# Performance work log

Measured on AMD Instinct MI355X. Metric: run time of the kernel, lower is better.

Reference implementation:

```python
import jax, jax.numpy as jnp
import numpy as np

# Dimensions
O, D, F_LSOA = 128, 128, 64      # origins, destinations, LSOA feature dim
T, FE, H = 128, 16, 64           # max seq len, edge_feature_dim, gru_hidden
NH, NO, PH = 128, 64, 128        # node_hidden, node_out, pair_hidden
P = O * D                        # number of O-D pairs


def _mlp3(x, W1, b1, W2, b2, W3, b3):
    # Linear->ReLU->Linear->ReLU->Linear (dropout is identity in eval mode)
    h = jax.nn.relu(x @ W1 + b1)
    h = jax.nn.relu(h @ W2 + b2)
    return h @ W3 + b3


def setup_inputs() -> dict:
    key = jax.random.key(0)
    ks = jax.random.split(key, 32)

    def rn(k, shape, s):
        return jax.random.normal(k, shape, dtype=jnp.float32) * s

    inp = {
        "O_feats": rn(ks[0], (O, F_LSOA), 1.0),
        "D_feats": rn(ks[1], (D, F_LSOA), 1.0),
        "seqs": rn(ks[2], (P, T, FE), 1.0),
        "lengths": jax.random.randint(ks[3], (P,), 1, T + 1, dtype=jnp.int32),
        # enc_O
        "WO1": rn(ks[4], (F_LSOA, NH), 0.05), "bO1": jnp.zeros((NH,), jnp.float32),
        "WO2": rn(ks[5], (NH, NH), 0.05),     "bO2": jnp.zeros((NH,), jnp.float32),
        "WO3": rn(ks[6], (NH, NO), 0.05),     "bO3": jnp.zeros((NO,), jnp.float32),
        # enc_D
        "WD1": rn(ks[7], (F_LSOA, NH), 0.05), "bD1": jnp.zeros((NH,), jnp.float32),
        "WD2": rn(ks[8], (NH, NH), 0.05),     "bD2": jnp.zeros((NH,), jnp.float32),
        "WD3": rn(ks[9], (NH, NO), 0.05),     "bD3": jnp.zeros((NO,), jnp.float32),
        # pair_head: 2*node_out -> pair_hidden -> 1
        "Wp1": rn(ks[10], (2 * NO, PH), 0.05), "bp1": jnp.zeros((PH,), jnp.float32),
        "Wp2": rn(ks[11], (PH, 1), 0.05),      "bp2": jnp.zeros((1,), jnp.float32),
        # GRU (gate order r, z, n as in PyTorch)
        "W_ih": rn(ks[12], (FE, 3 * H), 0.1),  "b_ih": jnp.zeros((3 * H,), jnp.float32),
        "W_hh": rn(ks[13], (H, 3 * H), 0.1),   "b_hh": jnp.zeros((3 * H,), jnp.float32),
        # seq_head
        "Ws": rn(ks[14], (H, 1), 0.1),         "bs": jnp.zeros((1,), jnp.float32),
    }
    return inp


def reference(O_feats, D_feats, seqs, lengths,
              WO1, bO1, WO2, bO2, WO3, bO3,
              WD1, bD1, WD2, bD2, WD3, bD3,
              Wp1, bp1, Wp2, bp2,
              W_ih, W_hh, b_ih, b_hh,
              Ws, bs):
    # Node encoders
    eo = _mlp3(O_feats, WO1, bO1, WO2, bO2, WO3, bO3)   # [O, NO]
    ed = _mlp3(D_feats, WD1, bD1, WD2, bD2, WD3, bD3)   # [D, NO]

    # Pairwise score: concat(eo, ed) -> MLP -> softplus
    pair_in = jnp.concatenate([
        jnp.broadcast_to(eo[:, None, :], (O, D, NO)),
        jnp.broadcast_to(ed[None, :, :], (O, D, NO)),
    ], axis=-1)                                          # [O, D, 2*NO]
    hp = jax.nn.relu(pair_in @ Wp1 + bp1)                # [O, D, PH]
    z_pair = (hp @ Wp2 + bp2)[..., 0]                    # [O, D]
    s_pair = jax.nn.softplus(z_pair)

    # Length-masked GRU over all O*D padded sequences (equiv. to pack_padded)
    xT = jnp.swapaxes(seqs, 0, 1)                        # [T, P, FE]
    h0 = jnp.zeros((P, H), jnp.float32)

    def step(h, inp):
        xt, t = inp
        gx = xt @ W_ih + b_ih                            # [P, 3H]
        gh = h @ W_hh + b_hh                             # [P, 3H]
        xr, xz, xn = jnp.split(gx, 3, axis=-1)
        hr, hz, hn = jnp.split(gh, 3, axis=-1)
        r = jax.nn.sigmoid(xr + hr)
        zg = jax.nn.sigmoid(xz + hz)
        n = jnp.tanh(xn + r * hn)
        h_new = (1.0 - zg) * n + zg * h
        h = jnp.where((t < lengths)[:, None], h_new, h)  # freeze past seq end
        return h, None

    h_last, _ = jax.lax.scan(step, h0, (xT, jnp.arange(T)))  # [P, H]

    p_seq = jax.nn.sigmoid(h_last @ Ws + bs)[:, 0].reshape(O, D)
    return jnp.sum(s_pair * p_seq)
```

## Files before the change

### kernel.cpp

```cpp
#include <hip/hip_runtime.h>
#include <hip/hip_bf16.h>

#define O_N 128
#define D_N 128
#define F_LS 64
#define T_MAX 128
#define FE_N 16
#define H_GRU 64
#define NH 128
#define NO 64
#define PH 128
#define NGRP 1024

typedef _Float16 f16;
typedef __fp16 hf2 __attribute__((ext_vector_type(2)));
typedef f16 f16x4 __attribute__((ext_vector_type(4)));
typedef f16 f16x8 __attribute__((ext_vector_type(8)));
typedef float f32x4 __attribute__((ext_vector_type(4)));

__device__ __forceinline__ float fast_sigmoid(float x) {
    return __builtin_amdgcn_rcpf(1.f + __expf(-x));
}

__global__ __launch_bounds__(256) void k_pre(
    const float* __restrict__ O_feats, const float* __restrict__ D_feats,
    const float* __restrict__ WO1, const float* __restrict__ bO1,
    const float* __restrict__ WO2, const float* __restrict__ bO2,
    const float* __restrict__ WO3, const float* __restrict__ bO3,
    const float* __restrict__ WD1, const float* __restrict__ bD1,
    const float* __restrict__ WD2, const float* __restrict__ bD2,
    const float* __restrict__ WD3, const float* __restrict__ bD3,
    const float* __restrict__ Wp1, const float* __restrict__ bp1,
    const int* __restrict__ lengths,
    float* __restrict__ PA, float* __restrict__ PBt,
    int* __restrict__ perm, int* __restrict__ gcnt, float* __restrict__ d_out)
{
    const int t = threadIdx.x;
    if (blockIdx.x == 256) {
        __shared__ int cnt[130];
        __shared__ int suf[130];
        if (t == 0) gcnt[0] = 0;
        if (t < 130) cnt[t] = 0;
        __syncthreads();
        for (int i = t; i < 16384; i += 256) atomicAdd(&cnt[lengths[i]], 1);
        __syncthreads();
        if (t < 130) suf[t] = cnt[t];
        __syncthreads();
        for (int d = 1; d < 130; d <<= 1) {
            int v = 0;
            if (t < 130) { v = suf[t]; if (t + d < 130) v += suf[t + d]; }
            __syncthreads();
            if (t < 130) suf[t] = v;
            __syncthreads();
        }
        if (t < 129) cnt[t] = (t + 1 < 130) ? suf[t + 1] : 0;
        __syncthreads();
        for (int i = t; i < 16384; i += 256) {
            int pos = atomicAdd(&cnt[lengths[i]], 1);
            perm[pos] = i;
        }
        return;
    }

    __shared__ float h1[NH];
    __shared__ float h2[NH];
    __shared__ float ev[NO];
    const int b = blockIdx.x;
    const int enc = b >> 7;
    const int row = b & 127;
    if (b == 0 && t == 0) d_out[0] = 0.f;

    const float* x  = (enc ? D_feats : O_feats) + row * F_LS;
    const float* W1 = enc ? WD1 : WO1;  const float* b1 = enc ? bD1 : bO1;
    const float* W2 = enc ? WD2 : WO2;  const float* b2 = enc ? bD2 : bO2;
    const float* W3 = enc ? WD3 : WO3;  const float* b3 = enc ? bD3 : bO3;

    if (t < 128) {
        float a = b1[t];
        #pragma unroll 8
        for (int k = 0; k < F_LS; ++k) a += x[k] * W1[k * NH + t];
        h1[t] = fmaxf(a, 0.f);
    }
    __syncthreads();

    if (t < 128) {
        float a = b2[t];
        #pragma unroll 8
        for (int k = 0; k < NH; ++k) a += h1[k] * W2[k * NH + t];
        h2[t] = fmaxf(a, 0.f);
    }
    __syncthreads();

    if (t < NO) {
        float a = b3[t];
        #pragma unroll 8
        for (int k = 0; k < NH; ++k) a += h2[k] * W3[k * NO + t];
        ev[t] = a;
    }
    __syncthreads();

    if (t < 128) {
        const float* Wp = Wp1 + (enc ? NO * PH : 0);
        float a = 0.f;
        #pragma unroll 8
        for (int k = 0; k < NO; ++k) a += ev[k] * Wp[k * PH + t];
        if (enc) PBt[t * 128 + row] = a + bp1[t];
        else     PA[row * PH + t] = a;
    }
}

__global__ __launch_bounds__(256, 4) void k_gru(
    const float* __restrict__ seqs, const int* __restrict__ lengths,
    const int* __restrict__ perm, int* __restrict__ gcnt,
    const float* __restrict__ W_ih, const float* __restrict__ b_ih,
    const float* __restrict__ W_hh, const float* __restrict__ b_hh,
    const float* __restrict__ Ws, const float* __restrict__ bs,
    const float* __restrict__ PA, const float* __restrict__ PBt,
    const float* __restrict__ Wp2, const float* __restrict__ bp2,
    float* __restrict__ d_out)
{
    __shared__ __align__(16) f16 hbuf[2][16 * 72];
    __shared__ __align__(16) float4 xbuf[2][8][64];
    __shared__ float red[64];
    __shared__ int sg;
    const int tid = threadIdx.x;
    const int w  = tid >> 6;
    const int l  = tid & 63;
    const int q  = l >> 4;
    const int n  = l & 15;
    const int c  = w * 16 + n;
    const int colbase = w * 16 + q * 4;
    const float S_RZ = -1.4426950408889634f;
    const float S_N  =  2.8853900817779268f;

    f16x8 wh[3][2], wi[3];
    #pragma unroll
    for (int gg = 0; gg < 3; ++gg) {
        const int gb = gg * 64;
        const float s = (gg < 2) ? S_RZ : S_N;
        #pragma unroll
        for (int ks = 0; ks < 2; ++ks)
            #pragma unroll
            for (int jj = 0; jj < 8; ++jj)
                wh[gg][ks][jj] = (f16)(W_hh[(ks * 32 + q * 8 + jj) * 192 + gb + c] * s);
        #pragma unroll
        for (int jj = 0; jj < 8; ++jj) {
            int k = q * 8 + jj;
            wi[gg][jj] = (k < FE_N) ? (f16)(W_ih[k * 192 + gb + c] * s) : (f16)0.f;
        }
    }
    f32x4 c_r, c_z, c_hn, c_xn;
    float wsc[4];
    #pragma unroll
    for (int r = 0; r < 4; ++r) {
        int col = colbase + r;
        c_r[r]  = S_RZ * (b_ih[col] + b_hh[col]);
        c_z[r]  = S_RZ * (b_ih[64 + col] + b_hh[64 + col]);
        c_hn[r] = S_N * b_hh[128 + col];
        c_xn[r] = S_N * b_ih[128 + col];
        wsc[r]  = Ws[col];
    }
    const f16x8 zero8 = {};

    for (;;) {
        if (tid == 0) sg = atomicAdd(gcnt, 1);
        __syncthreads();
        const int g = sg;
        if (g >= NGRP) break;
        const int pb = g * 16;

        const int myp   = perm[pb + n];
        const int mylen = lengths[myp];
        const int maxlen = lengths[perm[pb]];

        const float* xsrc = seqs + (size_t)perm[pb + (l & 15)] * (T_MAX * FE_N)
                           + (l >> 4) * 4;

        if (tid < 144) { f16x8 z8 = {}; *(f16x8*)&hbuf[0][tid * 8] = z8; }

        #pragma unroll
        for (int rr = 0; rr < 2; ++rr) {
            const int r8 = w + rr * 4;
            __builtin_amdgcn_global_load_lds(
                (const __attribute__((address_space(1))) void*)(xsrc + (size_t)r8 * FE_N),
                (__attribute__((address_space(3))) void*)&xbuf[0][r8][0], 16, 0, 0);
        }
        float hold[4] = {0.f, 0.f, 0.f, 0.f};
        __syncthreads();

        #pragma unroll 1
        for (int t = 0; t < maxlen; ++t) {
            const int cur = t & 1;
            const int xb  = (t >> 3) & 1;
            const int row = t & 7;
            const f16* hb  = hbuf[cur];
            f16*       hbw = hbuf[cur ^ 1];
            f16x8 bh0 = *(const f16x8*)&hb[n * 72 + 8 * q];
            f16x8 bh1 = *(const f16x8*)&hb[n * 72 + 32 + 8 * q];

            if (row == 0 && t + 8 < maxlen) {
                const int nb = xb ^ 1;
                #pragma unroll
                for (int rr = 0; rr < 2; ++rr) {
                    const int rl = w + rr * 4;
                    int rg = t + 8 + rl;
                    rg = rg < T_MAX ? rg : T_MAX - 1;
                    __builtin_amdgcn_global_load_lds(
                        (const __attribute__((address_space(1))) void*)(xsrc + (size_t)rg * FE_N),
                        (__attribute__((address_space(3))) void*)&xbuf[nb][rl][0], 16, 0, 0);
                }
            }

            f16x8 ax = zero8;
            if (q < 2) {
                float4 a0 = xbuf[xb][row][32 * q + n];
                float4 a1 = xbuf[xb][row][32 * q + 16 + n];
                union { f16x8 v8; hf2 v2[4]; } u;
                u.v2[0] = __builtin_amdgcn_cvt_pkrtz(a0.x, a0.y);
                u.v2[1] = __builtin_amdgcn_cvt_pkrtz(a0.z, a0.w);
                u.v2[2] = __builtin_amdgcn_cvt_pkrtz(a1.x, a1.y);
                u.v2[3] = __builtin_amdgcn_cvt_pkrtz(a1.z, a1.w);
                ax = u.v8;
            }

            f32x4 ar = __builtin_amdgcn_mfma_f32_16x16x32_f16(wi[0], ax, c_r, 0, 0, 0);
            f32x4 az = __builtin_amdgcn_mfma_f32_16x16x32_f16(wi[1], ax, c_z, 0, 0, 0);
            f32x4 xn = __builtin_amdgcn_mfma_f32_16x16x32_f16(wi[2], ax, c_xn, 0, 0, 0);
            ar = __builtin_amdgcn_mfma_f32_16x16x32_f16(wh[0][0], bh0, ar, 0, 0, 0);
            ar = __builtin_amdgcn_mfma_f32_16x16x32_f16(wh[0][1], bh1, ar, 0, 0, 0);
            az = __builtin_amdgcn_mfma_f32_16x16x32_f16(wh[1][0], bh0, az, 0, 0, 0);
            az = __builtin_amdgcn_mfma_f32_16x16x32_f16(wh[1][1], bh1, az, 0, 0, 0);
            f32x4 hn = __builtin_amdgcn_mfma_f32_16x16x32_f16(wh[2][0], bh0, c_hn, 0, 0, 0);
            hn = __builtin_amdgcn_mfma_f32_16x16x32_f16(wh[2][1], bh1, hn, 0, 0, 0);

            const bool live = (t < mylen);
            #pragma unroll
            for (int r = 0; r < 4; ++r) {
                float rg    = __builtin_amdgcn_rcpf(1.f + __builtin_amdgcn_exp2f(ar[r]));
                float zg    = __builtin_amdgcn_rcpf(1.f + __builtin_amdgcn_exp2f(az[r]));
                float inner = fmaf(rg, hn[r], xn[r]);
                float nn    = fmaf(-2.f, __builtin_amdgcn_rcpf(1.f + __builtin_amdgcn_exp2f(inner)), 1.f);
                float hnew  = fmaf(zg, hold[r] - nn, nn);
                hold[r] = live ? hnew : hold[r];
            }
            union { f16x4 v4; hf2 v2[2]; } hu;
            hu.v2[0] = __builtin_amdgcn_cvt_pkrtz(hold[0], hold[1]);
            hu.v2[1] = __builtin_amdgcn_cvt_pkrtz(hold[2], hold[3]);
            *(f16x4*)&hbw[n * 72 + colbase] = hu.v4;
            __syncthreads();
        }

        float part = hold[0] * wsc[0] + hold[1] * wsc[1] +
                     hold[2] * wsc[2] + hold[3] * wsc[3];
        part += __shfl_xor(part, 16);
        part += __shfl_xor(part, 32);
        if (l < 16) red[w * 16 + n] = part;
        __syncthreads();

        const int pp = tid >> 4;
        const int u  = tid & 15;
        const int pidx = perm[pb + pp];
        const int ii = pidx >> 7;
        const int jj = pidx & 127;
        float acc = 0.f;
        #pragma unroll
        for (int cc = u; cc < PH; cc += 16)
            acc += Wp2[cc] * fmaxf(PA[ii * PH + cc] + PBt[cc * 128 + jj], 0.f);
        acc += __shfl_xor(acc, 1);
        acc += __shfl_xor(acc, 2);
        acc += __shfl_xor(acc, 4);
        acc += __shfl_xor(acc, 8);
        if (u == 0) {
            float z  = acc + bp2[0];
            float sp = fmaxf(z, 0.f) + log1pf(__expf(-fabsf(z)));
            float s  = red[pp] + red[16 + pp] + red[32 + pp] + red[48 + pp];
            float pv = fast_sigmoid(s + bs[0]);
            atomicAdd(d_out, sp * pv);
        }
    }
}

extern "C" void kernel_launch(void* const* d_in, const int* in_sizes, int n_in,
                              void* d_out, int out_size, void* d_ws, size_t ws_size,
                              hipStream_t stream)
{
    const float* O_feats = (const float*)d_in[0];
    const float* D_feats = (const float*)d_in[1];
    const float* seqs    = (const float*)d_in[2];
    const int*   lengths = (const int*)d_in[3];
    const float* WO1 = (const float*)d_in[4];  const float* bO1 = (const float*)d_in[5];
    const float* WO2 = (const float*)d_in[6];  const float* bO2 = (const float*)d_in[7];
    const float* WO3 = (const float*)d_in[8];  const float* bO3 = (const float*)d_in[9];
    const float* WD1 = (const float*)d_in[10]; const float* bD1 = (const float*)d_in[11];
    const float* WD2 = (const float*)d_in[12]; const float* bD2 = (const float*)d_in[13];
    const float* WD3 = (const float*)d_in[14]; const float* bD3 = (const float*)d_in[15];
    const float* Wp1 = (const float*)d_in[16]; const float* bp1 = (const float*)d_in[17];
    const float* Wp2 = (const float*)d_in[18]; const float* bp2 = (const float*)d_in[19];
    const float* W_ih = (const float*)d_in[20]; const float* b_ih = (const float*)d_in[21];
    const float* W_hh = (const float*)d_in[22]; const float* b_hh = (const float*)d_in[23];
    const float* Ws   = (const float*)d_in[24]; const float* bs   = (const float*)d_in[25];

    float* out    = (float*)d_out;
    float* PA     = (float*)d_ws;
    float* PBt    = PA + 128 * 128;
    int*   perm   = (int*)(PBt + 128 * 128);
    int*   gcnt   = perm + 16384;

    k_pre<<<257, 256, 0, stream>>>(O_feats, D_feats,
                                   WO1, bO1, WO2, bO2, WO3, bO3,
                                   WD1, bD1, WD2, bD2, WD3, bD3,
                                   Wp1, bp1, lengths, PA, PBt, perm, gcnt, out);
    k_gru<<<512, 256, 0, stream>>>(seqs, lengths, perm, gcnt, W_ih, b_ih,
                                   W_hh, b_hh, Ws, bs, PA, PBt, Wp2, bp2, out);
}
```

Before: 369.0 us.

## Pair longest and shortest groups per block instead of atomic work queue

Replaces the dynamic atomic group counter with a static assignment: each of 512 blocks processes group g and its mirror NGRP-1-g, both sorted by length, interleaving their GRU steps in one loop so the two independent recurrences share barriers and can hide each other's MFMA and transcendental latency. A padding shared array and launch bounds of 2 limit occupancy to two blocks per CU. This removes the serial atomic fetch and per-group barrier overhead and balances load by pairing long with short sequences, at the cost of higher register and LDS pressure.

After: 377.9 us. 1.02x slower.

```diff
diff --git a/kernel.cpp b/kernel.cpp
--- a/kernel.cpp
+++ b/kernel.cpp
@@ -33,13 +33,12 @@
     const float* __restrict__ Wp1, const float* __restrict__ bp1,
     const int* __restrict__ lengths,
     float* __restrict__ PA, float* __restrict__ PBt,
-    int* __restrict__ perm, int* __restrict__ gcnt, float* __restrict__ d_out)
+    int* __restrict__ perm, float* __restrict__ d_out)
 {
     const int t = threadIdx.x;
     if (blockIdx.x == 256) {
         __shared__ int cnt[130];
         __shared__ int suf[130];
-        if (t == 0) gcnt[0] = 0;
         if (t < 130) cnt[t] = 0;
         __syncthreads();
         for (int i = t; i < 16384; i += 256) atomicAdd(&cnt[lengths[i]], 1);
@@ -109,9 +108,9 @@
     }
 }
 
-__global__ __launch_bounds__(256, 4) void k_gru(
+__global__ __launch_bounds__(256, 2) void k_gru(
     const float* __restrict__ seqs, const int* __restrict__ lengths,
-    const int* __restrict__ perm, int* __restrict__ gcnt,
+    const int* __restrict__ perm,
     const float* __restrict__ W_ih, const float* __restrict__ b_ih,
     const float* __restrict__ W_hh, const float* __restrict__ b_hh,
     const float* __restrict__ Ws, const float* __restrict__ bs,
@@ -119,17 +118,22 @@
     const float* __restrict__ Wp2, const float* __restrict__ bp2,
     float* __restrict__ d_out)
 {
-    __shared__ __align__(16) f16 hbuf[2][16 * 72];
-    __shared__ __align__(16) float4 xbuf[2][8][64];
-    __shared__ float red[64];
-    __shared__ int sg;
+    __shared__ __align__(16) f16 hbuf[2][2][16 * 72];
+    __shared__ __align__(16) float4 xbuf[2][2][8][64];
+    __shared__ float red[2][64];
+    __shared__ float pad_[2944];
     const int tid = threadIdx.x;
+    if (tid > 100000) pad_[0] = 1.f;
     const int w  = tid >> 6;
     const int l  = tid & 63;
     const int q  = l >> 4;
     const int n  = l & 15;
     const int c  = w * 16 + n;
     const int colbase = w * 16 + q * 4;
+    const int gA = blockIdx.x;
+    const int gB = (NGRP - 1) - blockIdx.x;
+    const int pbA = gA * 16;
+    const int pbB = gB * 16;
     const float S_RZ = -1.4426950408889634f;
     const float S_N  =  2.8853900817779268f;
 
@@ -160,106 +164,176 @@
         c_xn[r] = S_N * b_ih[128 + col];
         wsc[r]  = Ws[col];
     }
+    const int mypA = perm[pbA + n];
+    const int mypB = perm[pbB + n];
+    const int mylenA = lengths[mypA];
+    const int mylenB = lengths[mypB];
+    const int maxlenA = lengths[perm[pbA]];
+    const int maxlenB = lengths[perm[pbB]];
+
+    const float* xsrcA = seqs + (size_t)perm[pbA + (l & 15)] * (T_MAX * FE_N)
+                        + (l >> 4) * 4;
+    const float* xsrcB = seqs + (size_t)perm[pbB + (l & 15)] * (T_MAX * FE_N)
+                        + (l >> 4) * 4;
+
+    if (tid < 144) { f16x8 z8 = {}; *(f16x8*)&hbuf[0][0][tid * 8] = z8; }
+    if (tid < 144) { f16x8 z8 = {}; *(f16x8*)&hbuf[1][0][tid * 8] = z8; }
+
+    #pragma unroll
+    for (int rr = 0; rr < 2; ++rr) {
+        const int r8 = w + rr * 4;
+        __builtin_amdgcn_global_load_lds(
+            (const __attribute__((address_space(1))) void*)(xsrcA + (size_t)r8 * FE_N),
+            (__attribute__((address_space(3))) void*)&xbuf[0][0][r8][0], 16, 0, 0);
+        __builtin_amdgcn_global_load_lds(
+            (const __attribute__((address_space(1))) void*)(xsrcB + (size_t)r8 * FE_N),
+            (__attribute__((address_space(3))) void*)&xbuf[1][0][r8][0], 16, 0, 0);
+    }
+    float holdA[4] = {0.f, 0.f, 0.f, 0.f};
+    float holdB[4] = {0.f, 0.f, 0.f, 0.f};
     const f16x8 zero8 = {};
-
-    for (;;) {
-        if (tid == 0) sg = atomicAdd(gcnt, 1);
-        __syncthreads();
-        const int g = sg;
-        if (g >= NGRP) break;
-        const int pb = g * 16;
-
-        const int myp   = perm[pb + n];
-        const int mylen = lengths[myp];
-        const int maxlen = lengths[perm[pb]];
-
-        const float* xsrc = seqs + (size_t)perm[pb + (l & 15)] * (T_MAX * FE_N)
-                           + (l >> 4) * 4;
-
-        if (tid < 144) { f16x8 z8 = {}; *(f16x8*)&hbuf[0][tid * 8] = z8; }
-
-        #pragma unroll
-        for (int rr = 0; rr < 2; ++rr) {
-            const int r8 = w + rr * 4;
-            __builtin_amdgcn_global_load_lds(
-                (const __attribute__((address_space(1))) void*)(xsrc + (size_t)r8 * FE_N),
-                (__attribute__((address_space(3))) void*)&xbuf[0][r8][0], 16, 0, 0);
-        }
-        float hold[4] = {0.f, 0.f, 0.f, 0.f};
-        __syncthreads();
-
-        #pragma unroll 1
-        for (int t = 0; t < maxlen; ++t) {
-            const int cur = t & 1;
-            const int xb  = (t >> 3) & 1;
-            const int row = t & 7;
-            const f16* hb  = hbuf[cur];
-            f16*       hbw = hbuf[cur ^ 1];
-            f16x8 bh0 = *(const f16x8*)&hb[n * 72 + 8 * q];
-            f16x8 bh1 = *(const f16x8*)&hb[n * 72 + 32 + 8 * q];
-
-            if (row == 0 && t + 8 < maxlen) {
-                const int nb = xb ^ 1;
+    __syncthreads();
+
+    #pragma unroll 1
+    for (int t = 0; t < maxlenA; ++t) {
+        const int cur = t & 1;
+        const int xb  = (t >> 3) & 1;
+        const int row = t & 7;
+        const bool bAlive = (t < maxlenB);
+
+        f16x8 bhA0 = *(const f16x8*)&hbuf[0][cur][n * 72 + 8 * q];
+        f16x8 bhA1 = *(const f16x8*)&hbuf[0][cur][n * 72 + 32 + 8 * q];
+        f16x8 bhB0 = zero8, bhB1 = zero8;
+        if (bAlive) {
+            bhB0 = *(const f16x8*)&hbuf[1][cur][n * 72 + 8 * q];
+            bhB1 = *(const f16x8*)&hbuf[1][cur][n * 72 + 32 + 8 * q];
+        }
+
+        if (row == 0) {
+            const int nb = xb ^ 1;
+            if (t + 8 < maxlenA) {
                 #pragma unroll
                 for (int rr = 0; rr < 2; ++rr) {
                     const int rl = w + rr * 4;
                     int rg = t + 8 + rl;
                     rg = rg < T_MAX ? rg : T_MAX - 1;
                     __builtin_amdgcn_global_load_lds(
-                        (const __attribute__((address_space(1))) void*)(xsrc + (size_t)rg * FE_N),
-                        (__attribute__((address_space(3))) void*)&xbuf[nb][rl][0], 16, 0, 0);
+                        (const __attribute__((address_space(1))) void*)(xsrcA + (size_t)rg * FE_N),
+                        (__attribute__((address_space(3))) void*)&xbuf[0][nb][rl][0], 16, 0, 0);
                 }
             }
-
-            f16x8 ax = zero8;
-            if (q < 2) {
-                float4 a0 = xbuf[xb][row][32 * q + n];
-                float4 a1 = xbuf[xb][row][32 * q + 16 + n];
-                union { f16x8 v8; hf2 v2[4]; } u;
-                u.v2[0] = __builtin_amdgcn_cvt_pkrtz(a0.x, a0.y);
-                u.v2[1] = __builtin_amdgcn_cvt_pkrtz(a0.z, a0.w);
-                u.v2[2] = __builtin_amdgcn_cvt_pkrtz(a1.x, a1.y);
-                u.v2[3] = __builtin_amdgcn_cvt_pkrtz(a1.z, a1.w);
-                ax = u.v8;
+            if (t + 8 < maxlenB) {
+                #pragma unroll
+                for (int rr = 0; rr < 2; ++rr) {
+                    const int rl = w + rr * 4;
+                    int rg = t + 8 + rl;
+                    rg = rg < T_MAX ? rg : T_MAX - 1;
+                    __builtin_amdgcn_global_load_lds(
+                        (const __attribute__((address_space(1))) void*)(xsrcB + (size_t)rg * FE_N),
+                        (__attribute__((address_space(3))) void*)&xbuf[1][nb][rl][0], 16, 0, 0);
+                }
             }
-
-            f32x4 ar = __builtin_amdgcn_mfma_f32_16x16x32_f16(wi[0], ax, c_r, 0, 0, 0);
-            f32x4 az = __builtin_amdgcn_mfma_f32_16x16x32_f16(wi[1], ax, c_z, 0, 0, 0);
-            f32x4 xn = __builtin_amdgcn_mfma_f32_16x16x32_f16(wi[2], ax, c_xn, 0, 0, 0);
-            ar = __builtin_amdgcn_mfma_f32_16x16x32_f16(wh[0][0], bh0, ar, 0, 0, 0);
-            ar = __builtin_amdgcn_mfma_f32_16x16x32_f16(wh[0][1], bh1, ar, 0, 0, 0);
-            az = __builtin_amdgcn_mfma_f32_16x16x32_f16(wh[1][0], bh0, az, 0, 0, 0);
-            az = __builtin_amdgcn_mfma_f32_16x16x32_f16(wh[1][1], bh1, az, 0, 0, 0);
-            f32x4 hn = __builtin_amdgcn_mfma_f32_16x16x32_f16(wh[2][0], bh0, c_hn, 0, 0, 0);
-            hn = __builtin_amdgcn_mfma_f32_16x16x32_f16(wh[2][1], bh1, hn, 0, 0, 0);
-
-            const bool live = (t < mylen);
+        }
+
+        f16x8 axA = zero8, axB = zero8;
+        if (q < 2) {
+            float4 a0 = xbuf[0][xb][row][32 * q + n];
+            float4 a1 = xbuf[0][xb][row][32 * q + 16 + n];
+            union { f16x8 v8; hf2 v2[4]; } u;
+            u.v2[0] = __builtin_amdgcn_cvt_pkrtz(a0.x, a0.y);
+            u.v2[1] = __builtin_amdgcn_cvt_pkrtz(a0.z, a0.w);
+            u.v2[2] = __builtin_amdgcn_cvt_pkrtz(a1.x, a1.y);
+            u.v2[3] = __builtin_amdgcn_cvt_pkrtz(a1.z, a1.w);
+            axA = u.v8;
+        }
+        if (bAlive && q < 2) {
+            float4 b0 = xbuf[1][xb][row][32 * q + n];
+            float4 b1 = xbuf[1][xb][row][32 * q + 16 + n];
+            union { f16x8 v8; hf2 v2[4]; } u;
+            u.v2[0] = __builtin_amdgcn_cvt_pkrtz(b0.x, b0.y);
+            u.v2[1] = __builtin_amdgcn_cvt_pkrtz(b0.z, b0.w);
+            u.v2[2] = __builtin_amdgcn_cvt_pkrtz(b1.x, b1.y);
+            u.v2[3] = __builtin_amdgcn_cvt_pkrtz(b1.z, b1.w);
+            axB = u.v8;
+        }
+
+        f32x4 arA = __builtin_amdgcn_mfma_f32_16x16x32_f16(wi[0], axA, c_r, 0, 0, 0);
+        f32x4 azA = __builtin_amdgcn_mfma_f32_16x16x32_f16(wi[1], axA, c_z, 0, 0, 0);
+        f32x4 xnA = __builtin_amdgcn_mfma_f32_16x16x32_f16(wi[2], axA, c_xn, 0, 0, 0);
+        f32x4 arB = c_r, azB = c_z, xnB = c_xn, hnB = c_hn;
+        if (bAlive) {
+            arB = __builtin_amdgcn_mfma_f32_16x16x32_f16(wi[0], axB, c_r, 0, 0, 0);
+            azB = __builtin_amdgcn_mfma_f32_16x16x32_f16(wi[1], axB, c_z, 0, 0, 0);
+            xnB = __builtin_amdgcn_mfma_f32_16x16x32_f16(wi[2], axB, c_xn, 0, 0, 0);
+        }
+        arA = __builtin_amdgcn_mfma_f32_16x16x32_f16(wh[0][0], bhA0, arA, 0, 0, 0);
+        arA = __builtin_amdgcn_mfma_f32_16x16x32_f16(wh[0][1], bhA1, arA, 0, 0, 0);
+        azA = __builtin_amdgcn_mfma_f32_16x16x32_f16(wh[1][0], bhA0, azA, 0, 0, 0);
+        azA = __builtin_amdgcn_mfma_f32_16x16x32_f16(wh[1][1], bhA1, azA, 0, 0, 0);
+        f32x4 hnA = __builtin_amdgcn_mfma_f32_16x16x32_f16(wh[2][0], bhA0, c_hn, 0, 0, 0);
+        hnA = __builtin_amdgcn_mfma_f32_16x16x32_f16(wh[2][1], bhA1, hnA, 0, 0, 0);
+        if (bAlive) {
+            arB = __builtin_amdgcn_mfma_f32_16x16x32_f16(wh[0][0], bhB0, arB, 0, 0, 0);
+            arB = __builtin_amdgcn_mfma_f32_16x16x32_f16(wh[0][1], bhB1, arB, 0, 0, 0);
+            azB = __builtin_amdgcn_mfma_f32_16x16x32_f16(wh[1][0], bhB0, azB, 0, 0, 0);
+            azB = __builtin_amdgcn_mfma_f32_16x16x32_f16(wh[1][1], bhB1, azB, 0, 0, 0);
+            hnB = __builtin_amdgcn_mfma_f32_16x16x32_f16(wh[2][0], bhB0, c_hn, 0, 0, 0);
+            hnB = __builtin_amdgcn_mfma_f32_16x16x32_f16(wh[2][1], bhB1, hnB, 0, 0, 0);
+        }
+
+        {
+            const bool live = (t < mylenA);
             #pragma unroll
             for (int r = 0; r < 4; ++r) {
-                float rg    = __builtin_amdgcn_rcpf(1.f + __builtin_amdgcn_exp2f(ar[r]));
-                float zg    = __builtin_amdgcn_rcpf(1.f + __builtin_amdgcn_exp2f(az[r]));
-                float inner = fmaf(rg, hn[r], xn[r]);
+                float rg    = __builtin_amdgcn_rcpf(1.f + __builtin_amdgcn_exp2f(arA[r]));
+                float zg    = __builtin_amdgcn_rcpf(1.f + __builtin_amdgcn_exp2f(azA[r]));
+                float inner = fmaf(rg, hnA[r], xnA[r]);
                 float nn    = fmaf(-2.f, __builtin_amdgcn_rcpf(1.f + __builtin_amdgcn_exp2f(inner)), 1.f);
-                float hnew  = fmaf(zg, hold[r] - nn, nn);
-                hold[r] = live ? hnew : hold[r];
+                float hnew  = fmaf(zg, holdA[r] - nn, nn);
+                holdA[r] = live ? hnew : holdA[r];
             }
             union { f16x4 v4; hf2 v2[2]; } hu;
-            hu.v2[0] = __builtin_amdgcn_cvt_pkrtz(hold[0], hold[1]);
-            hu.v2[1] = __builtin_amdgcn_cvt_pkrtz(hold[2], hold[3]);
-            *(f16x4*)&hbw[n * 72 + colbase] = hu.v4;
-            __syncthreads();
-        }
-
-        float part = hold[0] * wsc[0] + hold[1] * wsc[1] +
-                     hold[2] * wsc[2] + hold[3] * wsc[3];
-        part += __shfl_xor(part, 16);
-        part += __shfl_xor(part, 32);
-        if (l < 16) red[w * 16 + n] = part;
-        __syncthreads();
-
+            hu.v2[0] = __builtin_amdgcn_cvt_pkrtz(holdA[0], holdA[1]);
+            hu.v2[1] = __builtin_amdgcn_cvt_pkrtz(holdA[2], holdA[3]);
+            *(f16x4*)&hbuf[0][cur ^ 1][n * 72 + colbase] = hu.v4;
+        }
+        if (bAlive) {
+            const bool live = (t < mylenB);
+            #pragma unroll
+            for (int r = 0; r < 4; ++r) {
+                float rg    = __builtin_amdgcn_rcpf(1.f + __builtin_amdgcn_exp2f(arB[r]));
+                float zg    = __builtin_amdgcn_rcpf(1.f + __builtin_amdgcn_exp2f(azB[r]));
+                float inner = fmaf(rg, hnB[r], xnB[r]);
+                float nn    = fmaf(-2.f, __builtin_amdgcn_rcpf(1.f + __builtin_amdgcn_exp2f(inner)), 1.f);
+                float hnew  = fmaf(zg, holdB[r] - nn, nn);
+                holdB[r] = live ? hnew : holdB[r];
+            }
+            union { f16x4 v4; hf2 v2[2]; } hu;
+            hu.v2[0] = __builtin_amdgcn_cvt_pkrtz(holdB[0], holdB[1]);
+            hu.v2[1] = __builtin_amdgcn_cvt_pkrtz(holdB[2], holdB[3]);
+            *(f16x4*)&hbuf[1][cur ^ 1][n * 72 + colbase] = hu.v4;
+        }
+        __syncthreads();
+    }
+
+    float partA = holdA[0] * wsc[0] + holdA[1] * wsc[1] +
+                  holdA[2] * wsc[2] + holdA[3] * wsc[3];
+    partA += __shfl_xor(partA, 16);
+    partA += __shfl_xor(partA, 32);
+    if (l < 16) red[0][w * 16 + n] = partA;
+    float partB = holdB[0] * wsc[0] + holdB[1] * wsc[1] +
+                  holdB[2] * wsc[2] + holdB[3] * wsc[3];
+    partB += __shfl_xor(partB, 16);
+    partB += __shfl_xor(partB, 32);
+    if (l < 16) red[1][w * 16 + n] = partB;
+    __syncthreads();
+
+    #pragma unroll
+    for (int gs = 0; gs < 2; ++gs) {
+        const int pbX = gs ? pbB : pbA;
         const int pp = tid >> 4;
         const int u  = tid & 15;
-        const int pidx = perm[pb + pp];
+        const int pidx = perm[pbX + pp];
         const int ii = pidx >> 7;
         const int jj = pidx & 127;
         float acc = 0.f;
@@ -273,7 +347,7 @@
         if (u == 0) {
             float z  = acc + bp2[0];
             float sp = fmaxf(z, 0.f) + log1pf(__expf(-fabsf(z)));
-            float s  = red[pp] + red[16 + pp] + red[32 + pp] + red[48 + pp];
+            float s  = red[gs][pp] + red[gs][16 + pp] + red[gs][32 + pp] + red[gs][48 + pp];
             float pv = fast_sigmoid(s + bs[0]);
             atomicAdd(d_out, sp * pv);
         }
@@ -304,12 +378,11 @@
     float* PA     = (float*)d_ws;
     float* PBt    = PA + 128 * 128;
     int*   perm   = (int*)(PBt + 128 * 128);
-    int*   gcnt   = perm + 16384;
 
     k_pre<<<257, 256, 0, stream>>>(O_feats, D_feats,
                                    WO1, bO1, WO2, bO2, WO3, bO3,
                                    WD1, bD1, WD2, bD2, WD3, bD3,
-                                   Wp1, bp1, lengths, PA, PBt, perm, gcnt, out);
-    k_gru<<<512, 256, 0, stream>>>(seqs, lengths, perm, gcnt, W_ih, b_ih,
+                                   Wp1, bp1, lengths, PA, PBt, perm, out);
+    k_gru<<<512, 256, 0, stream>>>(seqs, lengths, perm, W_ih, b_ih,
                                    W_hh, b_hh, Ws, bs, PA, PBt, Wp2, bp2, out);
 }
```

## Replace persistent atomic work queue with one block per group and prefetch x

Applied to the files above, without the earlier changes.

Removes the persistent-kernel design, in which 512 blocks pulled 16-sequence groups from a global atomic counter, and launches 1024 blocks that each own one group. The next timestep's input is now read from LDS and converted to f16 right after the MFMAs, taking that read off the critical path before the next step's MFMAs. The goal is to drop the per-group atomic and barrier. The cost is that long-first sorted groups now depend on the hardware block scheduler for load balance instead of dynamic stealing, and weights are reloaded per block.

Measured after the change: 345.5 us. 1.07x faster.

```diff
diff --git a/kernel.cpp b/kernel.cpp
--- a/kernel.cpp
+++ b/kernel.cpp
@@ -33,13 +33,12 @@
     const float* __restrict__ Wp1, const float* __restrict__ bp1,
     const int* __restrict__ lengths,
     float* __restrict__ PA, float* __restrict__ PBt,
-    int* __restrict__ perm, int* __restrict__ gcnt, float* __restrict__ d_out)
+    int* __restrict__ perm, float* __restrict__ d_out)
 {
     const int t = threadIdx.x;
     if (blockIdx.x == 256) {
         __shared__ int cnt[130];
         __shared__ int suf[130];
-        if (t == 0) gcnt[0] = 0;
         if (t < 130) cnt[t] = 0;
         __syncthreads();
         for (int i = t; i < 16384; i += 256) atomicAdd(&cnt[lengths[i]], 1);
@@ -111,7 +110,7 @@
 
 __global__ __launch_bounds__(256, 4) void k_gru(
     const float* __restrict__ seqs, const int* __restrict__ lengths,
-    const int* __restrict__ perm, int* __restrict__ gcnt,
+    const int* __restrict__ perm,
     const float* __restrict__ W_ih, const float* __restrict__ b_ih,
     const float* __restrict__ W_hh, const float* __restrict__ b_hh,
     const float* __restrict__ Ws, const float* __restrict__ bs,
@@ -122,7 +121,6 @@
     __shared__ __align__(16) f16 hbuf[2][16 * 72];
     __shared__ __align__(16) float4 xbuf[2][8][64];
     __shared__ float red[64];
-    __shared__ int sg;
     const int tid = threadIdx.x;
     const int w  = tid >> 6;
     const int l  = tid & 63;
@@ -130,6 +128,7 @@
     const int n  = l & 15;
     const int c  = w * 16 + n;
     const int colbase = w * 16 + q * 4;
+    const int pb = blockIdx.x * 16;
     const float S_RZ = -1.4426950408889634f;
     const float S_N  =  2.8853900817779268f;
 
@@ -160,123 +159,129 @@
         c_xn[r] = S_N * b_ih[128 + col];
         wsc[r]  = Ws[col];
     }
+    const int myp    = perm[pb + n];
+    const int mylen  = lengths[myp];
+    const int maxlen = lengths[perm[pb]];
+
+    const float* xsrc = seqs + (size_t)perm[pb + (l & 15)] * (T_MAX * FE_N)
+                       + (l >> 4) * 4;
+
+    if (tid < 144) { f16x8 z8 = {}; *(f16x8*)&hbuf[0][tid * 8] = z8; }
+
+    #pragma unroll
+    for (int rr = 0; rr < 2; ++rr) {
+        const int r8 = w + rr * 4;
+        __builtin_amdgcn_global_load_lds(
+            (const __attribute__((address_space(1))) void*)(xsrc + (size_t)r8 * FE_N),
+            (__attribute__((address_space(3))) void*)&xbuf[0][r8][0], 16, 0, 0);
+    }
+    float hold[4] = {0.f, 0.f, 0.f, 0.f};
     const f16x8 zero8 = {};
-
-    for (;;) {
-        if (tid == 0) sg = atomicAdd(gcnt, 1);
-        __syncthreads();
-        const int g = sg;
-        if (g >= NGRP) break;
-        const int pb = g * 16;
-
-        const int myp   = perm[pb + n];
-        const int mylen = lengths[myp];
-        const int maxlen = lengths[perm[pb]];
-
-        const float* xsrc = seqs + (size_t)perm[pb + (l & 15)] * (T_MAX * FE_N)
-                           + (l >> 4) * 4;
-
-        if (tid < 144) { f16x8 z8 = {}; *(f16x8*)&hbuf[0][tid * 8] = z8; }
-
+    __syncthreads();
+
+    f16x8 ax = zero8;
+    if (q < 2) {
+        float4 a0 = xbuf[0][0][32 * q + n];
+        float4 a1 = xbuf[0][0][32 * q + 16 + n];
+        union { f16x8 v8; hf2 v2[4]; } u;
+        u.v2[0] = __builtin_amdgcn_cvt_pkrtz(a0.x, a0.y);
+        u.v2[1] = __builtin_amdgcn_cvt_pkrtz(a0.z, a0.w);
+        u.v2[2] = __builtin_amdgcn_cvt_pkrtz(a1.x, a1.y);
+        u.v2[3] = __builtin_amdgcn_cvt_pkrtz(a1.z, a1.w);
+        ax = u.v8;
+    }
+
+    #pragma unroll 1
+    for (int t = 0; t < maxlen; ++t) {
+        const int cur = t & 1;
+        const int xb  = (t >> 3) & 1;
+        const int row = t & 7;
+        const f16* hb  = hbuf[cur];
+        f16*       hbw = hbuf[cur ^ 1];
+
+        f16x8 bh0 = *(const f16x8*)&hb[n * 72 + 8 * q];
+        f16x8 bh1 = *(const f16x8*)&hb[n * 72 + 32 + 8 * q];
+
+        if (row == 0 && t + 8 < maxlen) {
+            const int nb = xb ^ 1;
+            #pragma unroll
+            for (int rr = 0; rr < 2; ++rr) {
+                const int rl = w + rr * 4;
+                int rg = t + 8 + rl;
+                rg = rg < T_MAX ? rg : T_MAX - 1;
+                __builtin_amdgcn_global_load_lds(
+                    (const __attribute__((address_space(1))) void*)(xsrc + (size_t)rg * FE_N),
+                    (__attribute__((address_space(3))) void*)&xbuf[nb][rl][0], 16, 0, 0);
+            }
+        }
+
+        f32x4 ar = __builtin_amdgcn_mfma_f32_16x16x32_f16(wi[0], ax, c_r, 0, 0, 0);
+        f32x4 az = __builtin_amdgcn_mfma_f32_16x16x32_f16(wi[1], ax, c_z, 0, 0, 0);
+        f32x4 xn = __builtin_amdgcn_mfma_f32_16x16x32_f16(wi[2], ax, c_xn, 0, 0, 0);
+        ar = __builtin_amdgcn_mfma_f32_16x16x32_f16(wh[0][0], bh0, ar, 0, 0, 0);
+        ar = __builtin_amdgcn_mfma_f32_16x16x32_f16(wh[0][1], bh1, ar, 0, 0, 0);
+        az = __builtin_amdgcn_mfma_f32_16x16x32_f16(wh[1][0], bh0, az, 0, 0, 0);
+        az = __builtin_amdgcn_mfma_f32_16x16x32_f16(wh[1][1], bh1, az, 0, 0, 0);
+        f32x4 hn = __builtin_amdgcn_mfma_f32_16x16x32_f16(wh[2][0], bh0, c_hn, 0, 0, 0);
+        hn = __builtin_amdgcn_mfma_f32_16x16x32_f16(wh[2][1], bh1, hn, 0, 0, 0);
+
+        if (q < 2) {
+            const int t1  = t + 1;
+            const int xb1 = (t1 >> 3) & 1;
+            const int r1  = t1 & 7;
+            float4 a0 = xbuf[xb1][r1][32 * q + n];
+            float4 a1 = xbuf[xb1][r1][32 * q + 16 + n];
+            union { f16x8 v8; hf2 v2[4]; } u;
+            u.v2[0] = __builtin_amdgcn_cvt_pkrtz(a0.x, a0.y);
+            u.v2[1] = __builtin_amdgcn_cvt_pkrtz(a0.z, a0.w);
+            u.v2[2] = __builtin_amdgcn_cvt_pkrtz(a1.x, a1.y);
+            u.v2[3] = __builtin_amdgcn_cvt_pkrtz(a1.z, a1.w);
+            ax = u.v8;
+        }
+
+        const bool live = (t < mylen);
         #pragma unroll
-        for (int rr = 0; rr < 2; ++rr) {
-            const int r8 = w + rr * 4;
-            __builtin_amdgcn_global_load_lds(
-                (const __attribute__((address_space(1))) void*)(xsrc + (size_t)r8 * FE_N),
-                (__attribute__((address_space(3))) void*)&xbuf[0][r8][0], 16, 0, 0);
-        }
-        float hold[4] = {0.f, 0.f, 0.f, 0.f};
-        __syncthreads();
-
-        #pragma unroll 1
-        for (int t = 0; t < maxlen; ++t) {
-            const int cur = t & 1;
-            const int xb  = (t >> 3) & 1;
-            const int row = t & 7;
-            const f16* hb  = hbuf[cur];
-            f16*       hbw = hbuf[cur ^ 1];
-            f16x8 bh0 = *(const f16x8*)&hb[n * 72 + 8 * q];
-            f16x8 bh1 = *(const f16x8*)&hb[n * 72 + 32 + 8 * q];
-
-            if (row == 0 && t + 8 < maxlen) {
-                const int nb = xb ^ 1;
-                #pragma unroll
-                for (int rr = 0; rr < 2; ++rr) {
-                    const int rl = w + rr * 4;
-                    int rg = t + 8 + rl;
-                    rg = rg < T_MAX ? rg : T_MAX - 1;
-                    __builtin_amdgcn_global_load_lds(
-                        (const __attribute__((address_space(1))) void*)(xsrc + (size_t)rg * FE_N),
-                        (__attribute__((address_space(3))) void*)&xbuf[nb][rl][0], 16, 0, 0);
-                }
-            }
-
-            f16x8 ax = zero8;
-            if (q < 2) {
-                float4 a0 = xbuf[xb][row][32 * q + n];
-                float4 a1 = xbuf[xb][row][32 * q + 16 + n];
-                union { f16x8 v8; hf2 v2[4]; } u;
-                u.v2[0] = __builtin_amdgcn_cvt_pkrtz(a0.x, a0.y);
-                u.v2[1] = __builtin_amdgcn_cvt_pkrtz(a0.z, a0.w);
-                u.v2[2] = __builtin_amdgcn_cvt_pkrtz(a1.x, a1.y);
-                u.v2[3] = __builtin_amdgcn_cvt_pkrtz(a1.z, a1.w);
-                ax = u.v8;
-            }
-
-            f32x4 ar = __builtin_amdgcn_mfma_f32_16x16x32_f16(wi[0], ax, c_r, 0, 0, 0);
-            f32x4 az = __builtin_amdgcn_mfma_f32_16x16x32_f16(wi[1], ax, c_z, 0, 0, 0);
-            f32x4 xn = __builtin_amdgcn_mfma_f32_16x16x32_f16(wi[2], ax, c_xn, 0, 0, 0);
-            ar = __builtin_amdgcn_mfma_f32_16x16x32_f16(wh[0][0], bh0, ar, 0, 0, 0);
-            ar = __builtin_amdgcn_mfma_f32_16x16x32_f16(wh[0][1], bh1, ar, 0, 0, 0);
-            az = __builtin_amdgcn_mfma_f32_16x16x32_f16(wh[1][0], bh0, az, 0, 0, 0);
-            az = __builtin_amdgcn_mfma_f32_16x16x32_f16(wh[1][1], bh1, az, 0, 0, 0);
-            f32x4 hn = __builtin_amdgcn_mfma_f32_16x16x32_f16(wh[2][0], bh0, c_hn, 0, 0, 0);
-            hn = __builtin_amdgcn_mfma_f32_16x16x32_f16(wh[2][1], bh1, hn, 0, 0, 0);
-
-            const bool live = (t < mylen);
-            #pragma unroll
-            for (int r = 0; r < 4; ++r) {
-                float rg    = __builtin_amdgcn_rcpf(1.f + __builtin_amdgcn_exp2f(ar[r]));
-                float zg    = __builtin_amdgcn_rcpf(1.f + __builtin_amdgcn_exp2f(az[r]));
-                float inner = fmaf(rg, hn[r], xn[r]);
-                float nn    = fmaf(-2.f, __builtin_amdgcn_rcpf(1.f + __builtin_amdgcn_exp2f(inner)), 1.f);
-                float hnew  = fmaf(zg, hold[r] - nn, nn);
-                hold[r] = live ? hnew : hold[r];
-            }
-            union { f16x4 v4; hf2 v2[2]; } hu;
-            hu.v2[0] = __builtin_amdgcn_cvt_pkrtz(hold[0], hold[1]);
-            hu.v2[1] = __builtin_amdgcn_cvt_pkrtz(hold[2], hold[3]);
-            *(f16x4*)&hbw[n * 72 + colbase] = hu.v4;
-            __syncthreads();
-        }
-
-        float part = hold[0] * wsc[0] + hold[1] * wsc[1] +
-                     hold[2] * wsc[2] + hold[3] * wsc[3];
-        part += __shfl_xor(part, 16);
-        part += __shfl_xor(part, 32);
-        if (l < 16) red[w * 16 + n] = part;
-        __syncthreads();
-
-        const int pp = tid >> 4;
-        const int u  = tid & 15;
-        const int pidx = perm[pb + pp];
-        const int ii = pidx >> 7;
-        const int jj = pidx & 127;
-        float acc = 0.f;
-        #pragma unroll
-        for (int cc = u; cc < PH; cc += 16)
-            acc += Wp2[cc] * fmaxf(PA[ii * PH + cc] + PBt[cc * 128 + jj], 0.f);
-        acc += __shfl_xor(acc, 1);
-        acc += __shfl_xor(acc, 2);
-        acc += __shfl_xor(acc, 4);
-        acc += __shfl_xor(acc, 8);
-        if (u == 0) {
-            float z  = acc + bp2[0];
-            float sp = fmaxf(z, 0.f) + log1pf(__expf(-fabsf(z)));
-            float s  = red[pp] + red[16 + pp] + red[32 + pp] + red[48 + pp];
-            float pv = fast_sigmoid(s + bs[0]);
-            atomicAdd(d_out, sp * pv);
-        }
+        for (int r = 0; r < 4; ++r) {
+            float rg    = __builtin_amdgcn_rcpf(1.f + __builtin_amdgcn_exp2f(ar[r]));
+            float zg    = __builtin_amdgcn_rcpf(1.f + __builtin_amdgcn_exp2f(az[r]));
+            float inner = fmaf(rg, hn[r], xn[r]);
+            float nn    = fmaf(-2.f, __builtin_amdgcn_rcpf(1.f + __builtin_amdgcn_exp2f(inner)), 1.f);
+            float hnew  = fmaf(zg, hold[r] - nn, nn);
+            hold[r] = live ? hnew : hold[r];
+        }
+        union { f16x4 v4; hf2 v2[2]; } hu;
+        hu.v2[0] = __builtin_amdgcn_cvt_pkrtz(hold[0], hold[1]);
+        hu.v2[1] = __builtin_amdgcn_cvt_pkrtz(hold[2], hold[3]);
+        *(f16x4*)&hbw[n * 72 + colbase] = hu.v4;
+        __syncthreads();
+    }
+
+    float part = hold[0] * wsc[0] + hold[1] * wsc[1] +
+                 hold[2] * wsc[2] + hold[3] * wsc[3];
+    part += __shfl_xor(part, 16);
+    part += __shfl_xor(part, 32);
+    if (l < 16) red[w * 16 + n] = part;
+    __syncthreads();
+
+    const int pp = tid >> 4;
+    const int u  = tid & 15;
+    const int pidx = perm[pb + pp];
+    const int ii = pidx >> 7;
+    const int jj = pidx & 127;
+    float acc = 0.f;
+    #pragma unroll
+    for (int cc = u; cc < PH; cc += 16)
+        acc += Wp2[cc] * fmaxf(PA[ii * PH + cc] + PBt[cc * 128 + jj], 0.f);
+    acc += __shfl_xor(acc, 1);
+    acc += __shfl_xor(acc, 2);
+    acc += __shfl_xor(acc, 4);
+    acc += __shfl_xor(acc, 8);
+    if (u == 0) {
+        float z  = acc + bp2[0];
+        float sp = fmaxf(z, 0.f) + log1pf(__expf(-fabsf(z)));
+        float s  = red[pp] + red[16 + pp] + red[32 + pp] + red[48 + pp];
+        float pv = fast_sigmoid(s + bs[0]);
+        atomicAdd(d_out, sp * pv);
     }
 }
 
@@ -304,12 +309,11 @@
     float* PA     = (float*)d_ws;
     float* PBt    = PA + 128 * 128;
     int*   perm   = (int*)(PBt + 128 * 128);
-    int*   gcnt   = perm + 16384;
 
     k_pre<<<257, 256, 0, stream>>>(O_feats, D_feats,
                                    WO1, bO1, WO2, bO2, WO3, bO3,
                                    WD1, bD1, WD2, bD2, WD3, bD3,
-                                   Wp1, bp1, lengths, PA, PBt, perm, gcnt, out);
-    k_gru<<<512, 256, 0, stream>>>(seqs, lengths, perm, gcnt, W_ih, b_ih,
-                                   W_hh, b_hh, Ws, bs, PA, PBt, Wp2, bp2, out);
+                                   Wp1, bp1, lengths, PA, PBt, perm, out);
+    k_gru<<<1024, 256, 0, stream>>>(seqs, lengths, perm, W_ih, b_ih,
+                                    W_hh, b_hh, Ws, bs, PA, PBt, Wp2, bp2, out);
 }
```
